# Kernel tuning notes

Hardware: AMD Instinct MI355X
Metric: run time of the kernel (lower is better)

Reference implementation:

```python
import jax, jax.numpy as jnp
import numpy as np

B, C, H, W = 64, 512, 32, 32
N, K = 4, 1024          # num_codebooks, num_embeddings
D = C // N              # dims per codebook = 128


def setup_inputs() -> dict:
    key = jax.random.key(0)
    k1, k2 = jax.random.split(key)
    x = jax.random.normal(k1, (B, C, H, W), dtype=jnp.float32)
    embed = jax.random.normal(k2, (N, D, K), dtype=jnp.float32)  # codebooks
    return {"x": x, "embed": embed}


def reference(x, embed):
    """QLayer.up with downsample==1: identity encoder -> multi-codebook VQ.
    Returns (z_q [B,C,H,W], diff scalar, argmin [B,N,H,W], ppl scalar)."""
    P = B * H * W
    # channels-last, split channels into N codebooks of D dims each
    z = jnp.transpose(x, (0, 2, 3, 1)).reshape(P, N, D)          # [P,N,D]
    # squared L2 distance: ||z||^2 - 2 z.e + ||e||^2   -> [P,N,K]
    dist = (jnp.sum(z * z, axis=-1, keepdims=True)
            - 2.0 * jnp.einsum('pnd,ndk->pnk', z, embed)
            + jnp.sum(embed * embed, axis=1)[None])
    idx = jnp.argmin(dist, axis=-1)                              # [P,N] int
    # gather nearest codewords: embed_t [N,K,D]
    embed_t = jnp.transpose(embed, (0, 2, 1))
    q = embed_t[jnp.arange(N)[None, :], idx]                     # [P,N,D]
    q = q.reshape(B, H, W, C)
    z_bhwc = jnp.transpose(x, (0, 2, 3, 1))
    # commitment term and straight-through estimator
    diff = jnp.mean(jnp.square(jax.lax.stop_gradient(q) - z_bhwc))
    z_q = z_bhwc + jax.lax.stop_gradient(q - z_bhwc)
    z_q = jnp.transpose(z_q, (0, 3, 1, 2))                       # [B,C,H,W]
    # perplexity of codebook usage (mean over codebooks)
    counts = jnp.zeros((N, K), jnp.float32).at[
        jnp.broadcast_to(jnp.arange(N)[None, :], idx.shape), idx].add(1.0)
    probs = counts / P
    ppl = jnp.mean(jnp.exp(-jnp.sum(probs * jnp.log(probs + 1e-10), axis=-1)))
    argmin = jnp.transpose(idx.reshape(B, H, W, N), (0, 3, 1, 2))  # [B,N,H,W]
    return z_q, diff, argmin, ppl
```

## Files before the change

### kernel.cpp

```cpp
#include <hip/hip_runtime.h>
#include <math.h>

#define BB  64
#define CC  512
#define NN  4
#define KK  1024
#define DD  128
#define HW  1024
#define PP  65536

#define OFF_DIFF 33554432UL
#define OFF_ARG  33554433UL
#define OFF_PPL  33816577UL

#define WS_HIST   0
#define WS_DSUM   16384
#define WS_WLCNT  16392
#define WS_ENORM  16416
#define WS_EBF    32800
#define WS_EMBT   (32800 + 128*8192)
#define WS_WL     (WS_EMBT + NN*KK*DD*4)

#define DELTA 0.0625f

typedef _Float16 half8 __attribute__((ext_vector_type(8)));
typedef float f32x4 __attribute__((ext_vector_type(4)));

#define MFMA16(a, b, c) __builtin_amdgcn_mfma_f32_16x16x32_f16(a, b, c, 0, 0, 0)

__device__ __forceinline__ int swz(int row, int dbyte) {
    return (row * 256 + dbyte) ^ ((row & 15) << 4);
}
__device__ __forceinline__ void gl2lds16(const void* g, void* l) {
    __builtin_amdgcn_global_load_lds(
        (const __attribute__((address_space(1))) unsigned int*)g,
        (__attribute__((address_space(3))) unsigned int*)l, 16, 0, 0);
}

__global__ __launch_bounds__(256) void vq_prep(const float* __restrict__ embed,
                                               char* __restrict__ ebf,
                                               float* __restrict__ embt,
                                               float* __restrict__ enorm,
                                               unsigned* __restrict__ hist,
                                               double* __restrict__ dsum,
                                               unsigned* __restrict__ wlcnt) {
    __shared__ float sred[4][64];
    const int e = blockIdx.x, n = e >> 4, kt = e & 15, k0 = kt * 64;
    const int t = threadIdx.x, kr = t & 63, dc = t >> 6;
    if (t < 64) hist[e * 64 + t] = 0u;
    if (e == 0 && t == 0) { *dsum = 0.0; *wlcnt = 0u; }

    const float* src = embed + ((size_t)n * DD + dc * 32) * KK + k0 + kr;
    char* tile = ebf + ((size_t)(n * 32 + kt * 2 + (kr >> 5))) * 8192;
    const int row = kr & 31;
    float fv[32];
    #pragma unroll
    for (int r = 0; r < 32; ++r) fv[r] = src[(size_t)r * KK];
    float s = 0.f;
    #pragma unroll
    for (int j = 0; j < 4; ++j) {
        half8 vh;
        #pragma unroll
        for (int r = 0; r < 8; ++r) {
            float f = fv[j * 8 + r];
            vh[r] = (_Float16)f;
            s = fmaf(f, f, s);
        }
        *(half8*)(tile + swz(row, (dc * 32 + j * 8) * 2)) = vh;
    }
    {
        float* drow = embt + ((size_t)n * KK + k0 + kr) * DD + dc * 32;
        #pragma unroll
        for (int j = 0; j < 8; ++j)
            *(float4*)(drow + j * 4) = make_float4(fv[j*4], fv[j*4+1], fv[j*4+2], fv[j*4+3]);
    }
    sred[dc][kr] = s;
    __syncthreads();
    if (t < 64) enorm[n * KK + k0 + t] =
        -0.5f * ((sred[0][t] + sred[1][t]) + (sred[2][t] + sred[3][t]));
}

#define TOP2(C0, C1, MF, KP)                                                  \
    _Pragma("unroll")                                                         \
    for (int i_ = 0; i_ < 4; ++i_) {                                          \
        float v_ = C0[i_] + C1[i_];                                           \
        int r_ = (MF) * 4 + i_;                                               \
        float mn_ = fminf(pb1[r_], v_);                                       \
        pb2[r_] = fmaxf(pb2[r_], mn_);                                        \
        pk1[r_] = (v_ > pb1[r_]) ? (KP) : pk1[r_];                            \
        pb1[r_] = fmaxf(pb1[r_], v_);                                         \
    }

#define VSTEP(ACW, ACR, KTL, KPREV)                                           \
  {                                                                           \
    if (gW < 128) {                                                           \
        const char* s_ = ebf + (size_t)gW * 8192 + t * 16;                    \
        char* d_ = ebase + (bufW << 13) + t * 16;                             \
        gl2lds16(s_, d_);                                                     \
        gl2lds16(s_ + 4096, d_ + 4096);                                       \
    }                                                                         \
    ++gW; bufW = (bufW == 5) ? 0 : bufW + 1;                                  \
    const int rb_ = bufR << 13;                                               \
    bufR = (bufR == 5) ? 0 : bufR + 1;                                        \
    half8 bh0 = *(const half8*)(ebase + rb_ + bo0);                           \
    half8 bh1 = *(const half8*)(ebase + rb_ + bo1);                           \
    half8 bh2 = *(const half8*)(ebase + rb_ + bo2);                           \
    half8 bh3 = *(const half8*)(ebase + rb_ + bo3);                           \
    float e2a = enls[((KTL) << 5) + koff];                                    \
    f32x4 e2v = {e2a, e2a, e2a, e2a};                                         \
    ACW##00 = MFMA16(af[0][0], bh0, e2v);                                     \
    ACW##00 = MFMA16(af[0][1], bh1, ACW##00);                                 \
    ACW##01 = MFMA16(af[0][2], bh2, zz4);                                     \
    ACW##01 = MFMA16(af[0][3], bh3, ACW##01);                                 \
    ACW##10 = MFMA16(af[1][0], bh0, e2v);                                     \
    ACW##10 = MFMA16(af[1][1], bh1, ACW##10);                                 \
    ACW##11 = MFMA16(af[1][2], bh2, zz4);                                     \
    ACW##11 = MFMA16(af[1][3], bh3, ACW##11);                                 \
    TOP2(ACR##00, ACR##01, 0, KPREV);                                         \
    TOP2(ACR##10, ACR##11, 1, KPREV);                                         \
  }

__global__ __launch_bounds__(256, 2) void vq_main(const float* __restrict__ x,
                                                  const char* __restrict__ ebf,
                                                  const float* __restrict__ embt,
                                                  const float* __restrict__ enormg,
                                                  float* __restrict__ out,
                                                  unsigned* __restrict__ hist,
                                                  double* __restrict__ dsum,
                                                  unsigned* __restrict__ wlcnt,
                                                  int2* __restrict__ wl, int wlcap) {
    __shared__ __attribute__((aligned(16))) _Float16 zs[64 * 128];
    __shared__ __attribute__((aligned(16))) char ebuf[6][8192];
    __shared__ __attribute__((aligned(16))) float enls[KK];
    __shared__ int   idx_s[NN][64];
    __shared__ float red_b1[2][64], red_b2[2][64];
    __shared__ int   red_k1[2][64];
    __shared__ float wsum[4];

    const int t   = threadIdx.x;
    const int blk = blockIdx.x;
    const int b   = blk >> 4;
    const int hw0 = (blk & 15) << 6;
    const int w  = t >> 6, l = t & 63;
    const int pq = w >> 1;
    const int ks = w & 1;
    const int tk = l & 15, lg = l >> 4;
    const int koff = ks * 16 + tk;

    char* ebase = (char*)&ebuf[0][0];
    const int bo0 = swz(koff, (0 * 32 + lg * 8) * 2);
    const int bo1 = swz(koff, (1 * 32 + lg * 8) * 2);
    const int bo2 = swz(koff, (2 * 32 + lg * 8) * 2);
    const int bo3 = swz(koff, (3 * 32 + lg * 8) * 2);

    const f32x4 zz4 = {0.f, 0.f, 0.f, 0.f};
    const f32x4 m1e30 = {-1e30f, -1e30f, -1e30f, -1e30f};

    int bufR = 0, bufW = 4, gW = 4;
    float znacc = 0.f, sumb1 = 0.f;

    for (int n = 0; n < NN; ++n) {
        __syncthreads();
        gl2lds16((const char*)(enormg + n * KK) + t * 16, (char*)enls + t * 16);
        if (n == 0) {
            #pragma unroll
            for (int j = 0; j < 4; ++j) {
                const char* s_ = ebf + (size_t)j * 8192 + t * 16;
                char* d_ = ebase + j * 8192 + t * 16;
                gl2lds16(s_, d_);
                gl2lds16(s_ + 4096, d_ + 4096);
            }
        }
        {
            const int p = t & 63, dchunk = t >> 6;
            const float* xp = x + ((size_t)b * CC + n * DD + dchunk * 32) * HW + hw0 + p;
            float fv[32];
            #pragma unroll
            for (int r = 0; r < 32; ++r) fv[r] = xp[(size_t)r * HW];
            #pragma unroll
            for (int j = 0; j < 4; ++j) {
                half8 vh;
                #pragma unroll
                for (int r = 0; r < 8; ++r) {
                    float f = fv[j * 8 + r];
                    vh[r] = (_Float16)f;
                    znacc = fmaf(f, f, znacc);
                }
                *(half8*)((char*)zs + swz(p, (dchunk * 32 + j * 8) * 2)) = vh;
            }
        }
        __syncthreads();

        half8 af[2][4];
        #pragma unroll
        for (int mf = 0; mf < 2; ++mf)
            #pragma unroll
            for (int ds = 0; ds < 4; ++ds)
                af[mf][ds] = *(const half8*)((const char*)zs +
                               swz(pq * 32 + mf * 16 + tk, (ds * 32 + lg * 8) * 2));

        float pb1[8], pb2[8]; int pk1[8];
        #pragma unroll
        for (int r = 0; r < 8; ++r) { pb1[r] = -INFINITY; pb2[r] = -INFINITY; pk1[r] = 0; }

        f32x4 accA00, accA01, accA10, accA11;
        f32x4 accB00 = m1e30, accB01 = m1e30, accB10 = m1e30, accB11 = m1e30;

        #pragma unroll 1
        for (int wnd = 0; wnd < 16; ++wnd) {
            if (n == NN - 1 && wnd == 15)
                asm volatile("s_waitcnt vmcnt(0)" ::: "memory");
            else
                asm volatile("s_waitcnt vmcnt(4)" ::: "memory");
            __builtin_amdgcn_s_barrier();
            __builtin_amdgcn_sched_barrier(0);
            const int ka = wnd * 2;
            VSTEP(accA, accB, ka,     ((ka - 1) << 5) + koff)
            VSTEP(accB, accA, ka + 1, (ka << 5) + koff)
        }
        TOP2(accB00, accB01, 0, (31 << 5) + koff);
        TOP2(accB10, accB11, 1, (31 << 5) + koff);

        #pragma unroll
        for (int off = 1; off < 16; off <<= 1) {
            #pragma unroll
            for (int r = 0; r < 8; ++r) {
                float ob1 = __shfl_xor(pb1[r], off);
                float ob2 = __shfl_xor(pb2[r], off);
                int   ok1 = __shfl_xor(pk1[r], off);
                float nb2 = fmaxf(pb2[r], ob2);
                if (ob1 > pb1[r] || (ob1 == pb1[r] && ok1 < pk1[r])) {
                    pb2[r] = fmaxf(nb2, pb1[r]); pb1[r] = ob1; pk1[r] = ok1;
                } else {
                    pb2[r] = fmaxf(nb2, ob1);
                }
            }
        }
        if (tk == 0) {
            #pragma unroll
            for (int mf = 0; mf < 2; ++mf)
                #pragma unroll
                for (int i = 0; i < 4; ++i) {
                    int p = pq * 32 + mf * 16 + lg * 4 + i, r = mf * 4 + i;
                    red_b1[ks][p] = pb1[r]; red_b2[ks][p] = pb2[r]; red_k1[ks][p] = pk1[r];
                }
        }
        __syncthreads();
        if (t < 64) {
            int p = t;
            float m1 = red_b1[0][p], m2 = red_b2[0][p]; int mk = red_k1[0][p];
            {
                float ob1 = red_b1[1][p], ob2 = red_b2[1][p]; int ok = red_k1[1][p];
                float nb2 = fmaxf(m2, ob2);
                if (ob1 > m1 || (ob1 == m1 && ok < mk)) { m2 = fmaxf(nb2, m1); m1 = ob1; mk = ok; }
                else                                    { m2 = fmaxf(nb2, ob1); }
            }
            idx_s[n][p] = mk;
            atomicAdd(&hist[n * KK + mk], 1u);
            sumb1 += m1;
            if ((m1 - m2) < DELTA * 0.5f) {
                unsigned pos = atomicAdd(wlcnt, 1u);
                if ((int)pos < wlcap) wl[pos] = make_int2(b * HW + hw0 + p, n);
            }
        }
    }

    {
        float tot = znacc - 2.f * sumb1;
        #pragma unroll
        for (int off = 32; off > 0; off >>= 1) tot += __shfl_down(tot, off);
        if (l == 0) wsum[w] = tot;
        __syncthreads();
        if (t == 0) {
            double sd = 0.0;
            #pragma unroll
            for (int ww = 0; ww < 4; ++ww) sd += (double)wsum[ww];
            atomicAdd(dsum, sd);
        }
    }

    {
        int n2 = t >> 6, p = t & 63;
        out[OFF_ARG + (size_t)b * (NN * HW) + (size_t)n2 * HW + hw0 + p] = (float)idx_s[n2][p];
    }

    {
        const int p = t & 63, dchunk = t >> 6;
        #pragma unroll
        for (int n2 = 0; n2 < NN; ++n2) {
            int k = idx_s[n2][p];
            const float4* src = (const float4*)(embt + ((size_t)n2 * KK + k) * DD + dchunk * 32);
            const int c0 = n2 * 128 + dchunk * 32;
            #pragma unroll
            for (int r = 0; r < 8; ++r) {
                float4 q = src[r];
                out[((size_t)b * CC + c0 + r * 4 + 0) * HW + hw0 + p] = q.x;
                out[((size_t)b * CC + c0 + r * 4 + 1) * HW + hw0 + p] = q.y;
                out[((size_t)b * CC + c0 + r * 4 + 2) * HW + hw0 + p] = q.z;
                out[((size_t)b * CC + c0 + r * 4 + 3) * HW + hw0 + p] = q.w;
            }
        }
    }
}

#define ACCQ(U, V, J)                                                         \
  { double a0_ = (double)(V).x, a1_ = (double)(V).y,                          \
           a2_ = (double)(V).z, a3_ = (double)(V).w;                          \
    U = fma(a0_, zd2[(J)*4+0] - a0_, U);                                      \
    U = fma(a1_, zd2[(J)*4+1] - a1_, U);                                      \
    U = fma(a2_, zd2[(J)*4+2] - a2_, U);                                      \
    U = fma(a3_, zd2[(J)*4+3] - a3_, U); }

__global__ __launch_bounds__(256) void vq_refine(const float* __restrict__ x,
                                                 const float* __restrict__ embt,
                                                 float* __restrict__ out,
                                                 unsigned* __restrict__ hist,
                                                 const unsigned* __restrict__ wlcnt,
                                                 const int2* __restrict__ wl, int wlcap) {
    __shared__ float  zrow[DD];
    __shared__ double wbest[4];
    __shared__ int    wbestk[4];
    __shared__ int    flip_s;
    const int t = threadIdx.x;
    const int w = t >> 6, l = t & 63;
    const int rlane = l >> 3;
    const int dseg  = l & 7;

    unsigned wc = *wlcnt;
    int nitems = (int)(wc < (unsigned)wlcap ? wc : (unsigned)wlcap);

    for (int it = blockIdx.x; it < nitems; it += gridDim.x) {
        __syncthreads();
        int2 item = wl[it];
        int p = item.x, n = item.y;
        int b = p >> 10, hw = p & 1023;

        if (t < DD) zrow[t] = x[((size_t)b * CC + n * DD + t) * HW + hw];
        __syncthreads();

        double zd2[16];
        #pragma unroll
        for (int i = 0; i < 16; ++i) zd2[i] = 2.0 * (double)zrow[dseg * 16 + i];

        const float* en = embt + (size_t)n * KK * DD;
        double best = -INFINITY; int bestk = 0;
        const int rbase = w * 256;

        #pragma unroll 1
        for (int g0 = 0; g0 < 32; g0 += 2) {
            const int rowA = rbase + g0 * 8 + rlane;
            const int rowB = rowA + 8;
            const float4* erA = (const float4*)(en + (size_t)rowA * DD + dseg * 16);
            const float4* erB = (const float4*)(en + (size_t)rowB * DD + dseg * 16);
            float4 va0 = erA[0], va1 = erA[1], va2 = erA[2], va3 = erA[3];
            float4 vb0 = erB[0], vb1 = erB[1], vb2 = erB[2], vb3 = erB[3];
            double uA = 0.0, uB = 0.0;
            ACCQ(uA, va0, 0) ACCQ(uA, va1, 1) ACCQ(uA, va2, 2) ACCQ(uA, va3, 3)
            ACCQ(uB, vb0, 0) ACCQ(uB, vb1, 1) ACCQ(uB, vb2, 2) ACCQ(uB, vb3, 3)
            uA += __shfl_xor(uA, 1); uB += __shfl_xor(uB, 1);
            uA += __shfl_xor(uA, 2); uB += __shfl_xor(uB, 2);
            uA += __shfl_xor(uA, 4); uB += __shfl_xor(uB, 4);
            if (uA > best) { best = uA; bestk = rowA; }
            if (uB > best) { best = uB; bestk = rowB; }
        }
        #pragma unroll
        for (int mask = 8; mask <= 32; mask <<= 1) {
            double ob = __shfl_xor(best, mask);
            int    ok = __shfl_xor(bestk, mask);
            if (ob > best || (ob == best && ok < bestk)) { best = ob; bestk = ok; }
        }
        if (l == 0) { wbest[w] = best; wbestk[w] = bestk; }
        __syncthreads();
        if (t == 0) {
            double m = wbest[0]; int mk = wbestk[0];
            #pragma unroll
            for (int ww = 1; ww < 4; ++ww)
                if (wbest[ww] > m) { m = wbest[ww]; mk = wbestk[ww]; }
            size_t slot = OFF_ARG + (size_t)b * (NN * HW) + (size_t)n * HW + hw;
            int oldk = (int)out[slot];
            flip_s = -1;
            if (mk != oldk) {
                out[slot] = (float)mk;
                atomicSub(&hist[n * KK + oldk], 1u);
                atomicAdd(&hist[n * KK + mk], 1u);
                flip_s = mk;
            }
        }
        __syncthreads();
        int fk = flip_s;
        if (fk >= 0 && t < DD)
            out[((size_t)b * CC + n * DD + t) * HW + hw] = en[(size_t)fk * DD + t];
    }
}

__global__ __launch_bounds__(256) void vq_final(const unsigned* __restrict__ hist,
                                                const double* __restrict__ dsum,
                                                float* __restrict__ out) {
    __shared__ double red[256];
    __shared__ double hn[NN];
    const int t = threadIdx.x;
    for (int n = 0; n < NN; ++n) {
        double acc = 0.0;
        for (int k = t; k < KK; k += 256) {
            double pr = (double)hist[n * KK + k] / (double)PP;
            acc += pr * log(pr + 1e-10);
        }
        red[t] = acc;
        __syncthreads();
        for (int off = 128; off > 0; off >>= 1) {
            if (t < off) red[t] += red[t + off];
            __syncthreads();
        }
        if (t == 0) hn[n] = red[0];
        __syncthreads();
    }
    if (t == 0) {
        double ppl = 0.0;
        for (int n = 0; n < NN; ++n) ppl += exp(-hn[n]);
        out[OFF_PPL]  = (float)(ppl * 0.25);
        out[OFF_DIFF] = (float)(*dsum / (double)((size_t)BB * CC * HW));
    }
}

extern "C" void kernel_launch(void* const* d_in, const int* in_sizes, int n_in,
                              void* d_out, int out_size, void* d_ws, size_t ws_size,
                              hipStream_t stream) {
    const float* x     = (const float*)d_in[0];
    const float* embed = (const float*)d_in[1];
    float* out = (float*)d_out;
    char*  ws  = (char*)d_ws;

    unsigned* hist   = (unsigned*)(ws + WS_HIST);
    double*   dsum   = (double*)  (ws + WS_DSUM);
    unsigned* wlcnt  = (unsigned*)(ws + WS_WLCNT);
    float*    enorm  = (float*)   (ws + WS_ENORM);
    char*     ebf    = ws + WS_EBF;
    float*    embt   = (float*)   (ws + WS_EMBT);
    int2*     wl     = (int2*)    (ws + WS_WL);

    long long cap = ((long long)ws_size - WS_WL) / (long long)sizeof(int2);
    int wlcap = cap < 0 ? 0 : (cap > 65536 ? 65536 : (int)cap);

    vq_prep  <<<64,   256, 0, stream>>>(embed, ebf, embt, enorm, hist, dsum, wlcnt);
    vq_main  <<<1024, 256, 0, stream>>>(x, ebf, embt, enorm, out, hist, dsum, wlcnt, wl, wlcap);
    vq_refine<<<2048, 256, 0, stream>>>(x, embt, out, hist, wlcnt, wl, wlcap);
    vq_final <<<1,    256, 0, stream>>>(hist, dsum, out);
}
```

Baseline: 314.8 us.

## Double pixels per block to share codebook LDS tiles across 512 threads

vq_main now runs 512-thread blocks that each handle 128 pixels instead of 64. Every codebook tile streamed into LDS therefore serves twice as many pixels, which halves codebook global-to-LDS traffic per pixel and halves the grid size. The LDS ring shrinks from 6 to 4 buffers with prefetch distance 2, and each tile is loaded with a single 16-byte copy per thread and waited on at every step. The reduction arrays are aliased onto the zs buffer to save LDS, which needs an extra barrier. The shorter prefetch window and higher LDS use per block may expose more load latency or limit occupancy.

```diff
diff --git a/kernel.cpp b/kernel.cpp
--- a/kernel.cpp
+++ b/kernel.cpp
@@ -94,14 +94,11 @@
 #define VSTEP(ACW, ACR, KTL, KPREV)                                           \
   {                                                                           \
     if (gW < 128) {                                                           \
-        const char* s_ = ebf + (size_t)gW * 8192 + t * 16;                    \
-        char* d_ = ebase + (bufW << 13) + t * 16;                             \
-        gl2lds16(s_, d_);                                                     \
-        gl2lds16(s_ + 4096, d_ + 4096);                                       \
+        gl2lds16(ebf + (size_t)gW * 8192 + t * 16,                            \
+                 ebase + (gW & 3) * 8192 + t * 16);                           \
     }                                                                         \
-    ++gW; bufW = (bufW == 5) ? 0 : bufW + 1;                                  \
-    const int rb_ = bufR << 13;                                               \
-    bufR = (bufR == 5) ? 0 : bufR + 1;                                        \
+    ++gW;                                                                     \
+    const int rb_ = (((n << 5) + (KTL)) & 3) << 13;                           \
     half8 bh0 = *(const half8*)(ebase + rb_ + bo0);                           \
     half8 bh1 = *(const half8*)(ebase + rb_ + bo1);                           \
     half8 bh2 = *(const half8*)(ebase + rb_ + bo2);                           \
@@ -120,7 +117,12 @@
     TOP2(ACR##10, ACR##11, 1, KPREV);                                         \
   }
 
-__global__ __launch_bounds__(256, 2) void vq_main(const float* __restrict__ x,
+#define WAITBAR(WCNT)                                                         \
+    asm volatile("s_waitcnt vmcnt(" WCNT ")" ::: "memory");                   \
+    __builtin_amdgcn_s_barrier();                                             \
+    __builtin_amdgcn_sched_barrier(0);
+
+__global__ __launch_bounds__(512, 4) void vq_main(const float* __restrict__ x,
                                                   const char* __restrict__ ebf,
                                                   const float* __restrict__ embt,
                                                   const float* __restrict__ enormg,
@@ -129,18 +131,19 @@
                                                   double* __restrict__ dsum,
                                                   unsigned* __restrict__ wlcnt,
                                                   int2* __restrict__ wl, int wlcap) {
-    __shared__ __attribute__((aligned(16))) _Float16 zs[64 * 128];
-    __shared__ __attribute__((aligned(16))) char ebuf[6][8192];
+    __shared__ __attribute__((aligned(16))) _Float16 zs[128 * 128];
+    __shared__ __attribute__((aligned(16))) char ebuf[4][8192];
     __shared__ __attribute__((aligned(16))) float enls[KK];
-    __shared__ int   idx_s[NN][64];
-    __shared__ float red_b1[2][64], red_b2[2][64];
-    __shared__ int   red_k1[2][64];
-    __shared__ float wsum[4];
+    __shared__ int   idx_s[NN][128];
+    __shared__ float wsum[8];
+    float* red_b1 = (float*)zs;
+    float* red_b2 = (float*)((char*)zs + 1024);
+    int*   red_k1 = (int*)  ((char*)zs + 2048);
 
     const int t   = threadIdx.x;
     const int blk = blockIdx.x;
-    const int b   = blk >> 4;
-    const int hw0 = (blk & 15) << 6;
+    const int b   = blk >> 3;
+    const int hw0 = (blk & 7) << 7;
     const int w  = t >> 6, l = t & 63;
     const int pq = w >> 1;
     const int ks = w & 1;
@@ -156,23 +159,19 @@
     const f32x4 zz4 = {0.f, 0.f, 0.f, 0.f};
     const f32x4 m1e30 = {-1e30f, -1e30f, -1e30f, -1e30f};
 
-    int bufR = 0, bufW = 4, gW = 4;
+    int gW = 2;
     float znacc = 0.f, sumb1 = 0.f;
 
     for (int n = 0; n < NN; ++n) {
         __syncthreads();
-        gl2lds16((const char*)(enormg + n * KK) + t * 16, (char*)enls + t * 16);
+        if (t < 256)
+            gl2lds16((const char*)(enormg + n * KK) + t * 16, (char*)enls + t * 16);
         if (n == 0) {
-            #pragma unroll
-            for (int j = 0; j < 4; ++j) {
-                const char* s_ = ebf + (size_t)j * 8192 + t * 16;
-                char* d_ = ebase + j * 8192 + t * 16;
-                gl2lds16(s_, d_);
-                gl2lds16(s_ + 4096, d_ + 4096);
-            }
+            gl2lds16(ebf + (size_t)0 * 8192 + t * 16, ebase + t * 16);
+            gl2lds16(ebf + (size_t)1 * 8192 + t * 16, ebase + 8192 + t * 16);
         }
         {
-            const int p = t & 63, dchunk = t >> 6;
+            const int p = t & 127, dchunk = t >> 7;
             const float* xp = x + ((size_t)b * CC + n * DD + dchunk * 32) * HW + hw0 + p;
             float fv[32];
             #pragma unroll
@@ -207,16 +206,21 @@
         f32x4 accB00 = m1e30, accB01 = m1e30, accB10 = m1e30, accB11 = m1e30;
 
         #pragma unroll 1
-        for (int wnd = 0; wnd < 16; ++wnd) {
-            if (n == NN - 1 && wnd == 15)
-                asm volatile("s_waitcnt vmcnt(0)" ::: "memory");
-            else
-                asm volatile("s_waitcnt vmcnt(4)" ::: "memory");
-            __builtin_amdgcn_s_barrier();
-            __builtin_amdgcn_sched_barrier(0);
+        for (int wnd = 0; wnd < 15; ++wnd) {
             const int ka = wnd * 2;
+            WAITBAR("1")
             VSTEP(accA, accB, ka,     ((ka - 1) << 5) + koff)
+            WAITBAR("1")
             VSTEP(accB, accA, ka + 1, (ka << 5) + koff)
+        }
+        WAITBAR("1")
+        VSTEP(accA, accB, 30, (29 << 5) + koff)
+        if (n == NN - 1) {
+            WAITBAR("0")
+            VSTEP(accB, accA, 31, (30 << 5) + koff)
+        } else {
+            WAITBAR("1")
+            VSTEP(accB, accA, 31, (30 << 5) + koff)
         }
         TOP2(accB00, accB01, 0, (31 << 5) + koff);
         TOP2(accB10, accB11, 1, (31 << 5) + koff);
@@ -236,21 +240,24 @@
                 }
             }
         }
+        __syncthreads();
         if (tk == 0) {
             #pragma unroll
             for (int mf = 0; mf < 2; ++mf)
                 #pragma unroll
                 for (int i = 0; i < 4; ++i) {
                     int p = pq * 32 + mf * 16 + lg * 4 + i, r = mf * 4 + i;
-                    red_b1[ks][p] = pb1[r]; red_b2[ks][p] = pb2[r]; red_k1[ks][p] = pk1[r];
+                    red_b1[ks * 128 + p] = pb1[r];
+                    red_b2[ks * 128 + p] = pb2[r];
+                    red_k1[ks * 128 + p] = pk1[r];
                 }
         }
         __syncthreads();
-        if (t < 64) {
+        if (t < 128) {
             int p = t;
-            float m1 = red_b1[0][p], m2 = red_b2[0][p]; int mk = red_k1[0][p];
+            float m1 = red_b1[p], m2 = red_b2[p]; int mk = red_k1[p];
             {
-                float ob1 = red_b1[1][p], ob2 = red_b2[1][p]; int ok = red_k1[1][p];
+                float ob1 = red_b1[128 + p], ob2 = red_b2[128 + p]; int ok = red_k1[128 + p];
                 float nb2 = fmaxf(m2, ob2);
                 if (ob1 > m1 || (ob1 == m1 && ok < mk)) { m2 = fmaxf(nb2, m1); m1 = ob1; mk = ok; }
                 else                                    { m2 = fmaxf(nb2, ob1); }
@@ -274,18 +281,18 @@
         if (t == 0) {
             double sd = 0.0;
             #pragma unroll
-            for (int ww = 0; ww < 4; ++ww) sd += (double)wsum[ww];
+            for (int ww = 0; ww < 8; ++ww) sd += (double)wsum[ww];
             atomicAdd(dsum, sd);
         }
     }
 
     {
-        int n2 = t >> 6, p = t & 63;
+        int n2 = t >> 7, p = t & 127;
         out[OFF_ARG + (size_t)b * (NN * HW) + (size_t)n2 * HW + hw0 + p] = (float)idx_s[n2][p];
     }
 
     {
-        const int p = t & 63, dchunk = t >> 6;
+        const int p = t & 127, dchunk = t >> 7;
         #pragma unroll
         for (int n2 = 0; n2 < NN; ++n2) {
             int k = idx_s[n2][p];
@@ -442,7 +449,7 @@
     int wlcap = cap < 0 ? 0 : (cap > 65536 ? 65536 : (int)cap);
 
     vq_prep  <<<64,   256, 0, stream>>>(embed, ebf, embt, enorm, hist, dsum, wlcnt);
-    vq_main  <<<1024, 256, 0, stream>>>(x, ebf, embt, enorm, out, hist, dsum, wlcnt, wl, wlcap);
+    vq_main  <<<512,  512, 0, stream>>>(x, ebf, embt, enorm, out, hist, dsum, wlcnt, wl, wlcap);
     vq_refine<<<2048, 256, 0, stream>>>(x, embt, out, hist, wlcnt, wl, wlcap);
     vq_final <<<1,    256, 0, stream>>>(hist, dsum, out);
 }
```

Measured after the change: 385.3 us. +22.4%, slower.
